# Kernel optimization log

Hardware: AMD Instinct MI355X
Metric: run time of the kernel (lower is better)

Reference implementation:

```python
import jax, jax.numpy as jnp
import numpy as np

B, N, K = 4096, 16384, 512

def setup_inputs() -> dict:
    key = jax.random.key(0)
    x = jax.random.normal(key, (B, N), dtype=jnp.float32)
    return {"x": x, "k": K}

def reference(x, k):
    # Per-row abs top-k threshold + mask multiply (k < N assumed, matching config)
    Bsz = x.shape[0]
    flat = x.reshape(Bsz, -1)
    abs_flat = jnp.abs(flat)
    topk_vals, _ = jax.lax.top_k(abs_flat, k)          # [B, k]
    thresh = topk_vals[:, -1:]                          # [B, 1] kth largest abs value
    mask = (abs_flat >= thresh).astype(flat.dtype)
    return (flat * mask).reshape(x.shape)
```

## Files before the change

### kernel.cpp

```cpp
#include <hip/hip_runtime.h>

#define NTHREADS 256
#define ROWLEN 16384
#define PER_THREAD 16

template<int NB>
__device__ inline void select_bin(unsigned* hist, unsigned* wtot,
                                  unsigned* sel_bin, unsigned* sel_rem,
                                  unsigned tid, unsigned krem) {
  constexpr int BPT = NB / NTHREADS;
  const unsigned base = tid * BPT;
  unsigned c[BPT];
  unsigned s = 0;
#pragma unroll
  for (int i = 0; i < BPT; i++) { c[i] = hist[base + i]; s += c[i]; }

  const unsigned lane = tid & 63u;
  const unsigned wid  = tid >> 6;

  unsigned suf = s;
#pragma unroll
  for (int off = 1; off < 64; off <<= 1) {
    unsigned v = __shfl_down(suf, off);
    if (lane + off < 64) suf += v;
  }
  if (lane == 0) wtot[wid] = suf;
  __syncthreads();

  unsigned above = suf - s;
  for (unsigned w = wid + 1; w < 4; w++) above += wtot[w];

#pragma unroll
  for (int i = BPT - 1; i >= 0; i--) {
    unsigned cc = c[i];
    if (above < krem && above + cc >= krem) {
      *sel_bin = base + (unsigned)i;
      *sel_rem = krem - above;
    }
    above += cc;
  }
  __syncthreads();
}

__global__ __launch_bounds__(NTHREADS)
void topk_act_kernel(const float* __restrict__ x, float* __restrict__ out,
                     const int* __restrict__ kp) {
  __shared__ unsigned hist[2048];
  __shared__ unsigned wtot[4];
  __shared__ unsigned sel_bin, sel_rem;

  const unsigned tid = threadIdx.x;
  const unsigned k = (unsigned)*kp;
  const size_t rowoff = (size_t)blockIdx.x * (size_t)ROWLEN;
  const uint4* __restrict__ xr  = reinterpret_cast<const uint4*>(x + rowoff);
  uint4* __restrict__ orow      = reinterpret_cast<uint4*>(out + rowoff);

  uint4 d[PER_THREAD];
#pragma unroll
  for (int j = 0; j < PER_THREAD; j++) d[j] = xr[tid + j * NTHREADS];

#pragma unroll
  for (int i = 0; i < 2048 / NTHREADS; i++) hist[tid + i * NTHREADS] = 0u;
  __syncthreads();
#pragma unroll
  for (int j = 0; j < PER_THREAD; j++) {
    atomicAdd(&hist[(d[j].x & 0x7fffffffu) >> 20], 1u);
    atomicAdd(&hist[(d[j].y & 0x7fffffffu) >> 20], 1u);
    atomicAdd(&hist[(d[j].z & 0x7fffffffu) >> 20], 1u);
    atomicAdd(&hist[(d[j].w & 0x7fffffffu) >> 20], 1u);
  }
  __syncthreads();
  select_bin<2048>(hist, wtot, &sel_bin, &sel_rem, tid, k);
  const unsigned P1 = sel_bin;
  const unsigned r1 = sel_rem;
  __syncthreads();

#pragma unroll
  for (int i = 0; i < 1024 / NTHREADS; i++) hist[tid + i * NTHREADS] = 0u;
  __syncthreads();
#pragma unroll
  for (int j = 0; j < PER_THREAD; j++) {
    unsigned u;
    u = d[j].x & 0x7fffffffu; if ((u >> 20) == P1) atomicAdd(&hist[(u >> 10) & 0x3FFu], 1u);
    u = d[j].y & 0x7fffffffu; if ((u >> 20) == P1) atomicAdd(&hist[(u >> 10) & 0x3FFu], 1u);
    u = d[j].z & 0x7fffffffu; if ((u >> 20) == P1) atomicAdd(&hist[(u >> 10) & 0x3FFu], 1u);
    u = d[j].w & 0x7fffffffu; if ((u >> 20) == P1) atomicAdd(&hist[(u >> 10) & 0x3FFu], 1u);
  }
  __syncthreads();
  select_bin<1024>(hist, wtot, &sel_bin, &sel_rem, tid, r1);
  const unsigned P12 = (P1 << 10) | sel_bin;
  const unsigned r2 = sel_rem;
  __syncthreads();

#pragma unroll
  for (int i = 0; i < 1024 / NTHREADS; i++) hist[tid + i * NTHREADS] = 0u;
  __syncthreads();
#pragma unroll
  for (int j = 0; j < PER_THREAD; j++) {
    unsigned u;
    u = d[j].x & 0x7fffffffu; if ((u >> 10) == P12) atomicAdd(&hist[u & 0x3FFu], 1u);
    u = d[j].y & 0x7fffffffu; if ((u >> 10) == P12) atomicAdd(&hist[u & 0x3FFu], 1u);
    u = d[j].z & 0x7fffffffu; if ((u >> 10) == P12) atomicAdd(&hist[u & 0x3FFu], 1u);
    u = d[j].w & 0x7fffffffu; if ((u >> 10) == P12) atomicAdd(&hist[u & 0x3FFu], 1u);
  }
  __syncthreads();
  select_bin<1024>(hist, wtot, &sel_bin, &sel_rem, tid, r2);
  const unsigned V = (P12 << 10) | sel_bin;

#pragma unroll
  for (int j = 0; j < PER_THREAD; j++) {
    uint4 o;
    o.x = ((d[j].x & 0x7fffffffu) >= V) ? d[j].x : 0u;
    o.y = ((d[j].y & 0x7fffffffu) >= V) ? d[j].y : 0u;
    o.z = ((d[j].z & 0x7fffffffu) >= V) ? d[j].z : 0u;
    o.w = ((d[j].w & 0x7fffffffu) >= V) ? d[j].w : 0u;
    orow[tid + j * NTHREADS] = o;
  }
}

extern "C" void kernel_launch(void* const* d_in, const int* in_sizes, int n_in,
                              void* d_out, int out_size, void* d_ws, size_t ws_size,
                              hipStream_t stream) {
  const float* x  = (const float*)d_in[0];
  const int*   kp = (const int*)d_in[1];
  float*       out = (float*)d_out;
  const int rows = out_size / ROWLEN;
  topk_act_kernel<<<rows, NTHREADS, 0, stream>>>(x, out, kp);
}
```

Baseline: 444.6 us.

## Compact first-pass candidates into shared memory and widen block to 512 threads

After the first histogram pass, elements that fall in the selected top bin are appended to a shared candidate buffer. The second and third radix passes then scan only those candidates instead of every register-held element, with a fallback full scan if the buffer overflows. The block grows to 512 threads with 8 vectors each and gains an occupancy hint, and separate histograms remove the zeroing barriers between passes. The trade-offs are more shared memory per block and contention on a single atomic counter during compaction.

```diff
diff --git a/kernel.cpp b/kernel.cpp
--- a/kernel.cpp
+++ b/kernel.cpp
@@ -1,14 +1,15 @@
 #include <hip/hip_runtime.h>
 
-#define NTHREADS 256
+#define NT 512
 #define ROWLEN 16384
-#define PER_THREAD 16
+#define PT 8
+#define CAP 4096
 
 template<int NB>
 __device__ inline void select_bin(unsigned* hist, unsigned* wtot,
-                                  unsigned* sel_bin, unsigned* sel_rem,
-                                  unsigned tid, unsigned krem) {
-  constexpr int BPT = NB / NTHREADS;
+                                  unsigned* sel, unsigned tid, unsigned krem) {
+  constexpr int BPT = NB / NT;
+  constexpr int NW = NT / 64;
   const unsigned base = tid * BPT;
   unsigned c[BPT];
   unsigned s = 0;
@@ -28,102 +29,128 @@
   __syncthreads();
 
   unsigned above = suf - s;
-  for (unsigned w = wid + 1; w < 4; w++) above += wtot[w];
+  for (unsigned w = wid + 1; w < NW; w++) above += wtot[w];
 
 #pragma unroll
   for (int i = BPT - 1; i >= 0; i--) {
     unsigned cc = c[i];
     if (above < krem && above + cc >= krem) {
-      *sel_bin = base + (unsigned)i;
-      *sel_rem = krem - above;
+      sel[0] = base + (unsigned)i;
+      sel[1] = krem - above;
     }
     above += cc;
   }
   __syncthreads();
 }
 
-__global__ __launch_bounds__(NTHREADS)
+__global__ __launch_bounds__(NT, 6)
 void topk_act_kernel(const float* __restrict__ x, float* __restrict__ out,
                      const int* __restrict__ kp) {
-  __shared__ unsigned hist[2048];
-  __shared__ unsigned wtot[4];
-  __shared__ unsigned sel_bin, sel_rem;
+  __shared__ unsigned hist1[2048];
+  __shared__ unsigned hist2[1024];
+  __shared__ unsigned hist3[1024];
+  __shared__ unsigned cand[CAP];
+  __shared__ unsigned wtot[NT / 64];
+  __shared__ unsigned sel[2];
+  __shared__ unsigned cnt;
 
   const unsigned tid = threadIdx.x;
   const unsigned k = (unsigned)*kp;
   const size_t rowoff = (size_t)blockIdx.x * (size_t)ROWLEN;
-  const uint4* __restrict__ xr  = reinterpret_cast<const uint4*>(x + rowoff);
-  uint4* __restrict__ orow      = reinterpret_cast<uint4*>(out + rowoff);
+  const uint4* __restrict__ xr = reinterpret_cast<const uint4*>(x + rowoff);
+  uint4* __restrict__ orow     = reinterpret_cast<uint4*>(out + rowoff);
 
-  uint4 d[PER_THREAD];
+  uint4 d[PT];
 #pragma unroll
-  for (int j = 0; j < PER_THREAD; j++) d[j] = xr[tid + j * NTHREADS];
+  for (int j = 0; j < PT; j++) d[j] = xr[tid + j * NT];
 
 #pragma unroll
-  for (int i = 0; i < 2048 / NTHREADS; i++) hist[tid + i * NTHREADS] = 0u;
-  __syncthreads();
+  for (int i = 0; i < 2048 / NT; i++) hist1[tid + i * NT] = 0u;
 #pragma unroll
-  for (int j = 0; j < PER_THREAD; j++) {
-    atomicAdd(&hist[(d[j].x & 0x7fffffffu) >> 20], 1u);
-    atomicAdd(&hist[(d[j].y & 0x7fffffffu) >> 20], 1u);
-    atomicAdd(&hist[(d[j].z & 0x7fffffffu) >> 20], 1u);
-    atomicAdd(&hist[(d[j].w & 0x7fffffffu) >> 20], 1u);
-  }
-  __syncthreads();
-  select_bin<2048>(hist, wtot, &sel_bin, &sel_rem, tid, k);
-  const unsigned P1 = sel_bin;
-  const unsigned r1 = sel_rem;
+  for (int i = 0; i < 1024 / NT; i++) hist2[tid + i * NT] = 0u;
+#pragma unroll
+  for (int i = 0; i < 1024 / NT; i++) hist3[tid + i * NT] = 0u;
+  if (tid == 0) cnt = 0u;
   __syncthreads();
 
 #pragma unroll
-  for (int i = 0; i < 1024 / NTHREADS; i++) hist[tid + i * NTHREADS] = 0u;
-  __syncthreads();
-#pragma unroll
-  for (int j = 0; j < PER_THREAD; j++) {
-    unsigned u;
-    u = d[j].x & 0x7fffffffu; if ((u >> 20) == P1) atomicAdd(&hist[(u >> 10) & 0x3FFu], 1u);
-    u = d[j].y & 0x7fffffffu; if ((u >> 20) == P1) atomicAdd(&hist[(u >> 10) & 0x3FFu], 1u);
-    u = d[j].z & 0x7fffffffu; if ((u >> 20) == P1) atomicAdd(&hist[(u >> 10) & 0x3FFu], 1u);
-    u = d[j].w & 0x7fffffffu; if ((u >> 20) == P1) atomicAdd(&hist[(u >> 10) & 0x3FFu], 1u);
+  for (int j = 0; j < PT; j++) {
+    atomicAdd(&hist1[(d[j].x << 1) >> 21], 1u);
+    atomicAdd(&hist1[(d[j].y << 1) >> 21], 1u);
+    atomicAdd(&hist1[(d[j].z << 1) >> 21], 1u);
+    atomicAdd(&hist1[(d[j].w << 1) >> 21], 1u);
   }
   __syncthreads();
-  select_bin<1024>(hist, wtot, &sel_bin, &sel_rem, tid, r1);
-  const unsigned P12 = (P1 << 10) | sel_bin;
-  const unsigned r2 = sel_rem;
-  __syncthreads();
+  select_bin<2048>(hist1, wtot, sel, tid, k);
+  const unsigned P1 = sel[0];
+  const unsigned r1 = sel[1];
 
 #pragma unroll
-  for (int i = 0; i < 1024 / NTHREADS; i++) hist[tid + i * NTHREADS] = 0u;
-  __syncthreads();
-#pragma unroll
-  for (int j = 0; j < PER_THREAD; j++) {
-    unsigned u;
-    u = d[j].x & 0x7fffffffu; if ((u >> 10) == P12) atomicAdd(&hist[u & 0x3FFu], 1u);
-    u = d[j].y & 0x7fffffffu; if ((u >> 10) == P12) atomicAdd(&hist[u & 0x3FFu], 1u);
-    u = d[j].z & 0x7fffffffu; if ((u >> 10) == P12) atomicAdd(&hist[u & 0x3FFu], 1u);
-    u = d[j].w & 0x7fffffffu; if ((u >> 10) == P12) atomicAdd(&hist[u & 0x3FFu], 1u);
+  for (int j = 0; j < PT; j++) {
+    unsigned a;
+    a = d[j].x << 1; if ((a >> 21) == P1) { unsigned i = atomicAdd(&cnt, 1u); if (i < CAP) cand[i] = a; }
+    a = d[j].y << 1; if ((a >> 21) == P1) { unsigned i = atomicAdd(&cnt, 1u); if (i < CAP) cand[i] = a; }
+    a = d[j].z << 1; if ((a >> 21) == P1) { unsigned i = atomicAdd(&cnt, 1u); if (i < CAP) cand[i] = a; }
+    a = d[j].w << 1; if ((a >> 21) == P1) { unsigned i = atomicAdd(&cnt, 1u); if (i < CAP) cand[i] = a; }
   }
   __syncthreads();
-  select_bin<1024>(hist, wtot, &sel_bin, &sel_rem, tid, r2);
-  const unsigned V = (P12 << 10) | sel_bin;
+  const unsigned n = cnt;
+
+  if (n <= CAP) {
+    for (unsigned i = tid; i < n; i += NT)
+      atomicAdd(&hist2[(cand[i] >> 11) & 0x3FFu], 1u);
+  } else {
+#pragma unroll
+    for (int j = 0; j < PT; j++) {
+      unsigned a;
+      a = d[j].x << 1; if ((a >> 21) == P1) atomicAdd(&hist2[(a >> 11) & 0x3FFu], 1u);
+      a = d[j].y << 1; if ((a >> 21) == P1) atomicAdd(&hist2[(a >> 11) & 0x3FFu], 1u);
+      a = d[j].z << 1; if ((a >> 21) == P1) atomicAdd(&hist2[(a >> 11) & 0x3FFu], 1u);
+      a = d[j].w << 1; if ((a >> 21) == P1) atomicAdd(&hist2[(a >> 11) & 0x3FFu], 1u);
+    }
+  }
+  __syncthreads();
+  select_bin<1024>(hist2, wtot, sel, tid, r1);
+  const unsigned P2 = sel[0];
+  const unsigned r2 = sel[1];
+
+  if (n <= CAP) {
+    for (unsigned i = tid; i < n; i += NT) {
+      unsigned a = cand[i];
+      if (((a >> 11) & 0x3FFu) == P2) atomicAdd(&hist3[(a >> 1) & 0x3FFu], 1u);
+    }
+  } else {
+    const unsigned P12 = (P1 << 10) | P2;
+#pragma unroll
+    for (int j = 0; j < PT; j++) {
+      unsigned a;
+      a = d[j].x << 1; if ((a >> 11) == P12) atomicAdd(&hist3[(a >> 1) & 0x3FFu], 1u);
+      a = d[j].y << 1; if ((a >> 11) == P12) atomicAdd(&hist3[(a >> 1) & 0x3FFu], 1u);
+      a = d[j].z << 1; if ((a >> 11) == P12) atomicAdd(&hist3[(a >> 1) & 0x3FFu], 1u);
+      a = d[j].w << 1; if ((a >> 11) == P12) atomicAdd(&hist3[(a >> 1) & 0x3FFu], 1u);
+    }
+  }
+  __syncthreads();
+  select_bin<1024>(hist3, wtot, sel, tid, r2);
+  const unsigned Va = (P1 << 21) | (P2 << 11) | (sel[0] << 1);
 
 #pragma unroll
-  for (int j = 0; j < PER_THREAD; j++) {
+  for (int j = 0; j < PT; j++) {
     uint4 o;
-    o.x = ((d[j].x & 0x7fffffffu) >= V) ? d[j].x : 0u;
-    o.y = ((d[j].y & 0x7fffffffu) >= V) ? d[j].y : 0u;
-    o.z = ((d[j].z & 0x7fffffffu) >= V) ? d[j].z : 0u;
-    o.w = ((d[j].w & 0x7fffffffu) >= V) ? d[j].w : 0u;
-    orow[tid + j * NTHREADS] = o;
+    o.x = ((d[j].x << 1) >= Va) ? d[j].x : 0u;
+    o.y = ((d[j].y << 1) >= Va) ? d[j].y : 0u;
+    o.z = ((d[j].z << 1) >= Va) ? d[j].z : 0u;
+    o.w = ((d[j].w << 1) >= Va) ? d[j].w : 0u;
+    orow[tid + j * NT] = o;
   }
 }
 
 extern "C" void kernel_launch(void* const* d_in, const int* in_sizes, int n_in,
                               void* d_out, int out_size, void* d_ws, size_t ws_size,
                               hipStream_t stream) {
-  const float* x  = (const float*)d_in[0];
-  const int*   kp = (const int*)d_in[1];
+  const float* x   = (const float*)d_in[0];
+  const int*   kp  = (const int*)d_in[1];
   float*       out = (float*)d_out;
   const int rows = out_size / ROWLEN;
-  topk_act_kernel<<<rows, NTHREADS, 0, stream>>>(x, out, kp);
+  topk_act_kernel<<<rows, NT, 0, stream>>>(x, out, kp);
 }
```

New measurement: 443.0 us. No clear change (-0.4%).
